# Kernel optimization log

Measured on AMD Instinct MI355X. Metric: run time of the kernel, lower is better.

Reference implementation:

```python
import jax, jax.numpy as jnp
import numpy as np

N_HEAD = 16

def setup_inputs() -> dict:
    key = jax.random.key(0)
    ks = jax.random.split(key, 5)
    B, S, D = 2, 2048, 1024
    x = jax.random.normal(ks[0], (B, S, D), dtype=jnp.float32)
    w_attn = jax.random.normal(ks[1], (3 * D, D), dtype=jnp.float32) * 0.02
    b_attn = jax.random.normal(ks[2], (3 * D,), dtype=jnp.float32) * 0.02
    w_proj = jax.random.normal(ks[3], (D, D), dtype=jnp.float32) * 0.02
    b_proj = jax.random.normal(ks[4], (D,), dtype=jnp.float32) * 0.02
    return {"x": x, "w_attn": w_attn, "b_attn": b_attn, "w_proj": w_proj, "b_proj": b_proj}

def reference(x, w_attn, b_attn, w_proj, b_proj):
    B, S, D = x.shape
    H = N_HEAD
    hd = D // H
    # QKV projection (nn.Linear: x @ W^T + b)
    qkv = x @ w_attn.T + b_attn  # [B, S, 3D]
    q, k, v = jnp.split(qkv, 3, axis=2)
    q = q.reshape(B, S, H, hd).transpose(0, 2, 1, 3)  # [B, H, S, hd]
    k = k.reshape(B, S, H, hd).transpose(0, 2, 1, 3)
    v = v.reshape(B, S, H, hd).transpose(0, 2, 1, 3)
    scale = 1.0 / jnp.sqrt(jnp.asarray(hd, dtype=x.dtype))
    attn = jnp.einsum("bhqd,bhkd->bhqk", q, k) * scale  # [B, H, S, S]
    causal = jnp.tril(jnp.ones((S, S), dtype=bool))
    attn = jnp.where(causal[None, None], attn, -jnp.inf)
    attn = jax.nn.softmax(attn, axis=-1)
    y = jnp.einsum("bhqk,bhkd->bhqd", attn, v)  # [B, H, S, hd]
    y = y.transpose(0, 2, 1, 3).reshape(B, S, D)
    return y @ w_proj.T + b_proj
```

## Files before the change

### kernel.cpp

```cpp
#include <hip/hip_runtime.h>
#include <hip/hip_bf16.h>

#define S_LEN 2048
#define DMODEL 1024
#define NHEAD 16
#define HD 64

typedef short short8 __attribute__((ext_vector_type(8)));
typedef short short4_t __attribute__((ext_vector_type(4)));
typedef float f32x4 __attribute__((ext_vector_type(4)));

#define GLOAD_LDS16(gp, lp)                                        \
    __builtin_amdgcn_global_load_lds(                              \
        (__attribute__((address_space(1))) void*)(gp),             \
        (__attribute__((address_space(3))) void*)(lp), 16, 0, 0)

__device__ inline unsigned short f2bf(float f) {
    union { float f; unsigned int u; } c;
    c.f = f;
    unsigned int r = c.u + 0x7fffu + ((c.u >> 16) & 1u);
    return (unsigned short)(r >> 16);
}

__global__ __launch_bounds__(256) void cast_f32_bf16(
    const float* __restrict__ in, short* __restrict__ out, int n8)
{
    int i = blockIdx.x * 256 + threadIdx.x;
    if (i < n8) {
        float4 a = ((const float4*)in)[2 * i];
        float4 b = ((const float4*)in)[2 * i + 1];
        short8 o;
        o[0] = (short)f2bf(a.x); o[1] = (short)f2bf(a.y);
        o[2] = (short)f2bf(a.z); o[3] = (short)f2bf(a.w);
        o[4] = (short)f2bf(b.x); o[5] = (short)f2bf(b.y);
        o[6] = (short)f2bf(b.z); o[7] = (short)f2bf(b.w);
        ((short8*)out)[i] = o;
    }
}

template<bool QKV>
__global__ __launch_bounds__(256) void gemm_mfma(
    const short* __restrict__ A, const short* __restrict__ W,
    const float* __restrict__ bias, float* __restrict__ C,
    int N, int K,
    short* __restrict__ qo, short* __restrict__ ko, short* __restrict__ vo)
{
    __shared__ __align__(16) short Ash[128 * 64];
    __shared__ __align__(16) short Bsh[128 * 64];

    const int tid = threadIdx.x;
    const int l = tid & 63;
    const int wid = tid >> 6;
    const int wr = wid >> 1, wc = wid & 1;
    const int n0 = blockIdx.x << 7, m0 = blockIdx.y << 7;

    const short* Abase = A + (size_t)m0 * K;
    const short* Wbase = W + (size_t)n0 * K;

    f32x4 acc[4][4];
    #pragma unroll
    for (int i = 0; i < 4; ++i)
        #pragma unroll
        for (int j = 0; j < 4; ++j)
            acc[i][j] = (f32x4)0.0f;

    int rrow[4], scol[4];
    #pragma unroll
    for (int i = 0; i < 4; ++i) {
        int chunk = i * 256 + tid;
        rrow[i] = chunk >> 3;
        scol[i] = ((chunk & 7) ^ (rrow[i] & 7)) << 3;
    }

    const int NT = K >> 6;
    for (int kt = 0; kt < NT; ++kt) {
        const int k0 = kt << 6;
        __syncthreads();
        #pragma unroll
        for (int i = 0; i < 4; ++i) {
            GLOAD_LDS16(Abase + (size_t)rrow[i] * K + k0 + scol[i],
                        &Ash[(i * 256 + wid * 64) * 8]);
            GLOAD_LDS16(Wbase + (size_t)rrow[i] * K + k0 + scol[i],
                        &Bsh[(i * 256 + wid * 64) * 8]);
        }
        __syncthreads();
        #pragma unroll
        for (int kk = 0; kk < 2; ++kk) {
            short8 af[4], bf[4];
            const int slotg = (kk << 2) + (l >> 4);
            #pragma unroll
            for (int mi = 0; mi < 4; ++mi) {
                const int row = wr * 64 + mi * 16 + (l & 15);
                af[mi] = *(const short8*)&Ash[row * 64 + ((slotg ^ (row & 7)) << 3)];
            }
            #pragma unroll
            for (int ni = 0; ni < 4; ++ni) {
                const int row = wc * 64 + ni * 16 + (l & 15);
                bf[ni] = *(const short8*)&Bsh[row * 64 + ((slotg ^ (row & 7)) << 3)];
            }
            #pragma unroll
            for (int mi = 0; mi < 4; ++mi)
                #pragma unroll
                for (int ni = 0; ni < 4; ++ni)
                    acc[mi][ni] = __builtin_amdgcn_mfma_f32_16x16x32_bf16(
                        af[mi], bf[ni], acc[mi][ni], 0, 0, 0);
        }
    }

    #pragma unroll
    for (int ni = 0; ni < 4; ++ni) {
        const int col = n0 + wc * 64 + ni * 16 + (l & 15);
        const float bv = bias[col];
        if (QKV) {
            const int part = col >> 10;
            const int h = (col >> 6) & 15;
            const int e = col & 63;
            short* __restrict__ dst = part == 0 ? qo : (part == 1 ? ko : vo);
            #pragma unroll
            for (int mi = 0; mi < 4; ++mi) {
                #pragma unroll
                for (int r = 0; r < 4; ++r) {
                    int row = m0 + wr * 64 + mi * 16 + ((l >> 4) << 2) + r;
                    int b = row >> 11, s = row & (S_LEN - 1);
                    dst[((size_t)(b * NHEAD + h) * S_LEN + s) * HD + e] =
                        (short)f2bf(acc[mi][ni][r] + bv);
                }
            }
        } else {
            #pragma unroll
            for (int mi = 0; mi < 4; ++mi) {
                #pragma unroll
                for (int r = 0; r < 4; ++r) {
                    int row = m0 + wr * 64 + mi * 16 + ((l >> 4) << 2) + r;
                    C[(size_t)row * N + col] = acc[mi][ni][r] + bv;
                }
            }
        }
    }
}

__global__ __launch_bounds__(256) void transpose_v(
    const short* __restrict__ vin, short* __restrict__ vout)
{
    __shared__ short t[64][72];
    const int tid = threadIdx.x;
    const int bh = blockIdx.x >> 5;
    const int s0 = (blockIdx.x & 31) << 6;
    const size_t ibase = (size_t)bh * S_LEN * HD;
    const size_t obase = (size_t)bh * HD * S_LEN;
    const int r = tid >> 3, c8 = (tid & 7) << 3;

    #pragma unroll
    for (int p = 0; p < 2; ++p) {
        short8 v = *(const short8*)&vin[ibase + (size_t)(s0 + r + p * 32) * HD + c8];
        *(short8*)&t[r + p * 32][c8] = v;
    }
    __syncthreads();
    #pragma unroll
    for (int p = 0; p < 2; ++p) {
        const int e = r + p * 32;
        short8 o;
        #pragma unroll
        for (int i = 0; i < 8; ++i) o[i] = t[c8 + i][e];
        *(short8*)&vout[obase + (size_t)e * S_LEN + s0 + c8] = o;
    }
}

__global__ __launch_bounds__(256) void flash_attn_mfma(
    const short* __restrict__ q, const short* __restrict__ k,
    const short* __restrict__ vt, short* __restrict__ yb)
{
    __shared__ __align__(16) short Ks[64 * 64];
    __shared__ __align__(16) short Vs[64 * 64];

    const int tid = threadIdx.x;
    const int l = tid & 63;
    const int w = tid >> 6;
    const int h4 = l >> 4;
    const int c15 = l & 15;
    const int bid = blockIdx.x;
    const int qt = 31 - (bid >> 5);
    const int bh = bid & 31;
    const int q0 = qt << 6;
    const int myq = q0 + (w << 4) + c15;

    const size_t kbase = (size_t)bh * S_LEN * HD;
    const size_t vbase = (size_t)bh * HD * S_LEN;

    short8 qf[2];
    {
        const short* qrow = q + kbase + (size_t)myq * HD;
        qf[0] = *(const short8*)(qrow + (h4 << 3));
        qf[1] = *(const short8*)(qrow + 32 + (h4 << 3));
    }

    f32x4 accO[4];
    #pragma unroll
    for (int i = 0; i < 4; ++i) accO[i] = (f32x4)0.0f;
    float mr = -1e30f, lr = 0.0f;

    const int sr = tid >> 3, slotL = tid & 7;

    const int ntiles = qt + 1;
    for (int t = 0; t < ntiles; ++t) {
        const int kn = t << 6;
        __syncthreads();
        #pragma unroll
        for (int p = 0; p < 2; ++p) {
            const int row = sr + p * 32;
            const int ss = (slotL ^ (row & 7)) << 3;
            GLOAD_LDS16(k + kbase + (size_t)(kn + row) * HD + ss,
                        &Ks[(p * 256 + w * 64) * 8]);
            GLOAD_LDS16(vt + vbase + (size_t)row * S_LEN + kn + ss,
                        &Vs[(p * 256 + w * 64) * 8]);
        }
        __syncthreads();

        f32x4 sacc[4];
        #pragma unroll
        for (int nt = 0; nt < 4; ++nt) sacc[nt] = (f32x4)0.0f;
        #pragma unroll
        for (int c = 0; c < 2; ++c) {
            const int kof = (c << 5) + (h4 << 3);
            #pragma unroll
            for (int nt = 0; nt < 4; ++nt) {
                const int keyrow = nt * 16 + c15;
                const short8 kf = *(const short8*)&Ks[keyrow * 64 + (kof ^ ((keyrow & 7) << 3))];
                sacc[nt] = __builtin_amdgcn_mfma_f32_16x16x32_bf16(kf, qf[c], sacc[nt], 0, 0, 0);
            }
        }

        float p16[16];
        const bool diag = (t == qt);
        #pragma unroll
        for (int nt = 0; nt < 4; ++nt)
            #pragma unroll
            for (int r = 0; r < 4; ++r) {
                float v = sacc[nt][r] * 0.125f;
                if (diag && (nt * 16 + (h4 << 2) + r > (w << 4) + c15))
                    v = -1e30f;
                p16[nt * 4 + r] = v;
            }

        float mx = p16[0];
        #pragma unroll
        for (int i = 1; i < 16; ++i) mx = fmaxf(mx, p16[i]);
        mx = fmaxf(mx, __shfl_xor(mx, 16, 64));
        mx = fmaxf(mx, __shfl_xor(mx, 32, 64));
        if (!__all(mx <= mr)) {
            const float mnew = fmaxf(mr, mx);
            const float alpha = __expf(mr - mnew);
            mr = mnew;
            lr *= alpha;
            #pragma unroll
            for (int et = 0; et < 4; ++et) accO[et] *= alpha;
        }
        float rs = 0.0f;
        #pragma unroll
        for (int i = 0; i < 16; ++i) {
            p16[i] = __expf(p16[i] - mr);
            rs += p16[i];
        }
        rs += __shfl_xor(rs, 16, 64);
        rs += __shfl_xor(rs, 32, 64);
        lr += rs;

        short8 pb[2];
        #pragma unroll
        for (int c = 0; c < 2; ++c)
            #pragma unroll
            for (int i = 0; i < 8; ++i)
                pb[c][i] = (short)f2bf(p16[8 * c + i]);

        #pragma unroll
        for (int c = 0; c < 2; ++c) {
            const int ch = (c << 2) + (h4 >> 1);
            const int halfo = (h4 & 1) << 2;
            #pragma unroll
            for (int et = 0; et < 4; ++et) {
                const int e = (et << 4) + c15;
                const int rb = e << 6;
                const int sw = e & 7;
                const short4_t va = *(const short4_t*)&Vs[rb + ((ch ^ sw) << 3) + halfo];
                const short4_t vb = *(const short4_t*)&Vs[rb + (((ch + 2) ^ sw) << 3) + halfo];
                const short8 vf = {va[0], va[1], va[2], va[3], vb[0], vb[1], vb[2], vb[3]};
                accO[et] = __builtin_amdgcn_mfma_f32_16x16x32_bf16(vf, pb[c], accO[et], 0, 0, 0);
            }
        }
    }

    const int bq = bh >> 4, hh = bh & 15;
    const float inv = 1.0f / lr;
    short* orow = yb + ((size_t)bq * S_LEN + myq) * DMODEL + hh * HD;
    #pragma unroll
    for (int et = 0; et < 4; ++et) {
        short4_t o;
        #pragma unroll
        for (int r = 0; r < 4; ++r) o[r] = (short)f2bf(accO[et][r] * inv);
        *(short4_t*)&orow[(et << 4) + (h4 << 2)] = o;
    }
}

extern "C" void kernel_launch(void* const* d_in, const int* in_sizes, int n_in,
                              void* d_out, int out_size, void* d_ws, size_t ws_size,
                              hipStream_t stream) {
    const float* x      = (const float*)d_in[0];
    const float* w_attn = (const float*)d_in[1];
    const float* b_attn = (const float*)d_in[2];
    const float* w_proj = (const float*)d_in[3];
    const float* b_proj = (const float*)d_in[4];
    float* out = (float*)d_out;

    const int B = 2;
    const int M = B * S_LEN;
    const size_t x_elems  = (size_t)M * DMODEL;
    const size_t wa_elems = (size_t)3 * DMODEL * DMODEL;
    const size_t wp_elems = (size_t)DMODEL * DMODEL;

    char* wsb = (char*)d_ws;
    short* qw  = (short*)(wsb);
    short* kw  = (short*)(wsb + (8u << 20));
    short* vw  = (short*)(wsb + (16u << 20));
    short* vtw = (short*)(wsb + (24u << 20));
    short* xb  = (short*)(wsb + (32u << 20));
    short* yb  = (short*)(wsb + (32u << 20));
    short* wab = (short*)(wsb + (40u << 20));
    short* wpb = (short*)(wsb + (40u << 20));

    cast_f32_bf16<<<dim3((int)(x_elems  / 8 / 256)), 256, 0, stream>>>(x, xb, (int)(x_elems / 8));
    cast_f32_bf16<<<dim3((int)(wa_elems / 8 / 256)), 256, 0, stream>>>(w_attn, wab, (int)(wa_elems / 8));

    dim3 g1(3 * DMODEL / 128, M / 128);
    gemm_mfma<true><<<g1, 256, 0, stream>>>(xb, wab, b_attn, nullptr,
                                            3 * DMODEL, DMODEL, qw, kw, vw);

    cast_f32_bf16<<<dim3((int)(wp_elems / 8 / 256)), 256, 0, stream>>>(w_proj, wpb, (int)(wp_elems / 8));
    transpose_v<<<dim3(2 * NHEAD * (S_LEN / 64)), 256, 0, stream>>>(vw, vtw);

    flash_attn_mfma<<<dim3(2 * NHEAD * (S_LEN / 64)), 256, 0, stream>>>(qw, kw, vtw, yb);

    dim3 g3(DMODEL / 128, M / 128);
    gemm_mfma<false><<<g3, 256, 0, stream>>>(yb, wpb, b_proj, out,
                                             DMODEL, DMODEL,
                                             nullptr, nullptr, nullptr);
}
```

Measured before the change: 203.9 us.

## Double-buffer LDS in GEMM and flash attention, merge cast kernels

Both the GEMM and the flash-attention kernels now use two LDS buffers. The next K tile is loaded with global_load_lds while the current tile is computed, and the loop drops to one barrier per iteration. The three fp32-to-bf16 cast launches are merged into one kernel that routes each thread by index range, and w_proj gets its own workspace slot. LDS use doubles, which may lower occupancy, and the prefetched loads may not complete before the barrier without an explicit vmcnt wait.

After: 196.5 us. 3.6% less time.

```diff
diff --git a/kernel.cpp b/kernel.cpp
--- a/kernel.cpp
+++ b/kernel.cpp
@@ -22,20 +22,25 @@
     return (unsigned short)(r >> 16);
 }
 
-__global__ __launch_bounds__(256) void cast_f32_bf16(
-    const float* __restrict__ in, short* __restrict__ out, int n8)
+__global__ __launch_bounds__(256) void cast3_f32_bf16(
+    const float* __restrict__ x, const float* __restrict__ wa,
+    const float* __restrict__ wp,
+    short* __restrict__ xb, short* __restrict__ wab, short* __restrict__ wpb)
 {
-    int i = blockIdx.x * 256 + threadIdx.x;
-    if (i < n8) {
-        float4 a = ((const float4*)in)[2 * i];
-        float4 b = ((const float4*)in)[2 * i + 1];
-        short8 o;
-        o[0] = (short)f2bf(a.x); o[1] = (short)f2bf(a.y);
-        o[2] = (short)f2bf(a.z); o[3] = (short)f2bf(a.w);
-        o[4] = (short)f2bf(b.x); o[5] = (short)f2bf(b.y);
-        o[6] = (short)f2bf(b.z); o[7] = (short)f2bf(b.w);
-        ((short8*)out)[i] = o;
-    }
+    const int i = blockIdx.x * 256 + threadIdx.x;
+    const float* src;
+    short* dst;
+    if (i < 524288)      { src = x  + (size_t)i * 8;            dst = xb  + (size_t)i * 8; }
+    else if (i < 917504) { src = wa + (size_t)(i - 524288) * 8; dst = wab + (size_t)(i - 524288) * 8; }
+    else                 { src = wp + (size_t)(i - 917504) * 8; dst = wpb + (size_t)(i - 917504) * 8; }
+    float4 a = ((const float4*)src)[0];
+    float4 b = ((const float4*)src)[1];
+    short8 o;
+    o[0] = (short)f2bf(a.x); o[1] = (short)f2bf(a.y);
+    o[2] = (short)f2bf(a.z); o[3] = (short)f2bf(a.w);
+    o[4] = (short)f2bf(b.x); o[5] = (short)f2bf(b.y);
+    o[6] = (short)f2bf(b.z); o[7] = (short)f2bf(b.w);
+    *(short8*)dst = o;
 }
 
 template<bool QKV>
@@ -45,8 +50,8 @@
     int N, int K,
     short* __restrict__ qo, short* __restrict__ ko, short* __restrict__ vo)
 {
-    __shared__ __align__(16) short Ash[128 * 64];
-    __shared__ __align__(16) short Bsh[128 * 64];
+    __shared__ __align__(16) short Ash[2][128 * 64];
+    __shared__ __align__(16) short Bsh[2][128 * 64];
 
     const int tid = threadIdx.x;
     const int l = tid & 63;
@@ -72,18 +77,17 @@
         scol[i] = ((chunk & 7) ^ (rrow[i] & 7)) << 3;
     }
 
-    const int NT = K >> 6;
-    for (int kt = 0; kt < NT; ++kt) {
-        const int k0 = kt << 6;
-        __syncthreads();
+    auto stage = [&](int buf, int k0) {
         #pragma unroll
         for (int i = 0; i < 4; ++i) {
             GLOAD_LDS16(Abase + (size_t)rrow[i] * K + k0 + scol[i],
-                        &Ash[(i * 256 + wid * 64) * 8]);
+                        &Ash[buf][(i * 256 + wid * 64) * 8]);
             GLOAD_LDS16(Wbase + (size_t)rrow[i] * K + k0 + scol[i],
-                        &Bsh[(i * 256 + wid * 64) * 8]);
-        }
-        __syncthreads();
+                        &Bsh[buf][(i * 256 + wid * 64) * 8]);
+        }
+    };
+
+    auto compute = [&](int buf) {
         #pragma unroll
         for (int kk = 0; kk < 2; ++kk) {
             short8 af[4], bf[4];
@@ -91,12 +95,12 @@
             #pragma unroll
             for (int mi = 0; mi < 4; ++mi) {
                 const int row = wr * 64 + mi * 16 + (l & 15);
-                af[mi] = *(const short8*)&Ash[row * 64 + ((slotg ^ (row & 7)) << 3)];
+                af[mi] = *(const short8*)&Ash[buf][row * 64 + ((slotg ^ (row & 7)) << 3)];
             }
             #pragma unroll
             for (int ni = 0; ni < 4; ++ni) {
                 const int row = wc * 64 + ni * 16 + (l & 15);
-                bf[ni] = *(const short8*)&Bsh[row * 64 + ((slotg ^ (row & 7)) << 3)];
+                bf[ni] = *(const short8*)&Bsh[buf][row * 64 + ((slotg ^ (row & 7)) << 3)];
             }
             #pragma unroll
             for (int mi = 0; mi < 4; ++mi)
@@ -105,6 +109,17 @@
                     acc[mi][ni] = __builtin_amdgcn_mfma_f32_16x16x32_bf16(
                         af[mi], bf[ni], acc[mi][ni], 0, 0, 0);
         }
+    };
+
+    const int NT = K >> 6;
+    stage(0, 0);
+    __syncthreads();
+    int cur = 0;
+    for (int kt = 0; kt < NT; ++kt) {
+        if (kt + 1 < NT) stage(cur ^ 1, (kt + 1) << 6);
+        compute(cur);
+        __syncthreads();
+        cur ^= 1;
     }
 
     #pragma unroll
@@ -170,8 +185,8 @@
     const short* __restrict__ q, const short* __restrict__ k,
     const short* __restrict__ vt, short* __restrict__ yb)
 {
-    __shared__ __align__(16) short Ks[64 * 64];
-    __shared__ __align__(16) short Vs[64 * 64];
+    __shared__ __align__(16) short Ks[2][64 * 64];
+    __shared__ __align__(16) short Vs[2][64 * 64];
 
     const int tid = threadIdx.x;
     const int l = tid & 63;
@@ -201,20 +216,25 @@
 
     const int sr = tid >> 3, slotL = tid & 7;
 
-    const int ntiles = qt + 1;
-    for (int t = 0; t < ntiles; ++t) {
-        const int kn = t << 6;
-        __syncthreads();
+    auto stageKV = [&](int buf, int kn) {
         #pragma unroll
         for (int p = 0; p < 2; ++p) {
             const int row = sr + p * 32;
             const int ss = (slotL ^ (row & 7)) << 3;
             GLOAD_LDS16(k + kbase + (size_t)(kn + row) * HD + ss,
-                        &Ks[(p * 256 + w * 64) * 8]);
+                        &Ks[buf][(p * 256 + w * 64) * 8]);
             GLOAD_LDS16(vt + vbase + (size_t)row * S_LEN + kn + ss,
-                        &Vs[(p * 256 + w * 64) * 8]);
-        }
-        __syncthreads();
+                        &Vs[buf][(p * 256 + w * 64) * 8]);
+        }
+    };
+
+    const int ntiles = qt + 1;
+    stageKV(0, 0);
+    __syncthreads();
+    int cur = 0;
+
+    for (int t = 0; t < ntiles; ++t) {
+        if (t + 1 < ntiles) stageKV(cur ^ 1, (t + 1) << 6);
 
         f32x4 sacc[4];
         #pragma unroll
@@ -225,7 +245,7 @@
             #pragma unroll
             for (int nt = 0; nt < 4; ++nt) {
                 const int keyrow = nt * 16 + c15;
-                const short8 kf = *(const short8*)&Ks[keyrow * 64 + (kof ^ ((keyrow & 7) << 3))];
+                const short8 kf = *(const short8*)&Ks[cur][keyrow * 64 + (kof ^ ((keyrow & 7) << 3))];
                 sacc[nt] = __builtin_amdgcn_mfma_f32_16x16x32_bf16(kf, qf[c], sacc[nt], 0, 0, 0);
             }
         }
@@ -281,12 +301,15 @@
                 const int e = (et << 4) + c15;
                 const int rb = e << 6;
                 const int sw = e & 7;
-                const short4_t va = *(const short4_t*)&Vs[rb + ((ch ^ sw) << 3) + halfo];
-                const short4_t vb = *(const short4_t*)&Vs[rb + (((ch + 2) ^ sw) << 3) + halfo];
+                const short4_t va = *(const short4_t*)&Vs[cur][rb + ((ch ^ sw) << 3) + halfo];
+                const short4_t vb = *(const short4_t*)&Vs[cur][rb + (((ch + 2) ^ sw) << 3) + halfo];
                 const short8 vf = {va[0], va[1], va[2], va[3], vb[0], vb[1], vb[2], vb[3]};
                 accO[et] = __builtin_amdgcn_mfma_f32_16x16x32_bf16(vf, pb[c], accO[et], 0, 0, 0);
             }
         }
+
+        __syncthreads();
+        cur ^= 1;
     }
 
     const int bq = bh >> 4, hh = bh & 15;
@@ -313,9 +336,6 @@
 
     const int B = 2;
     const int M = B * S_LEN;
-    const size_t x_elems  = (size_t)M * DMODEL;
-    const size_t wa_elems = (size_t)3 * DMODEL * DMODEL;
-    const size_t wp_elems = (size_t)DMODEL * DMODEL;
 
     char* wsb = (char*)d_ws;
     short* qw  = (short*)(wsb);
@@ -325,16 +345,14 @@
     short* xb  = (short*)(wsb + (32u << 20));
     short* yb  = (short*)(wsb + (32u << 20));
     short* wab = (short*)(wsb + (40u << 20));
-    short* wpb = (short*)(wsb + (40u << 20));
-
-    cast_f32_bf16<<<dim3((int)(x_elems  / 8 / 256)), 256, 0, stream>>>(x, xb, (int)(x_elems / 8));
-    cast_f32_bf16<<<dim3((int)(wa_elems / 8 / 256)), 256, 0, stream>>>(w_attn, wab, (int)(wa_elems / 8));
+    short* wpb = (short*)(wsb + (46u << 20));
+
+    cast3_f32_bf16<<<dim3(4096), 256, 0, stream>>>(x, w_attn, w_proj, xb, wab, wpb);
 
     dim3 g1(3 * DMODEL / 128, M / 128);
     gemm_mfma<true><<<g1, 256, 0, stream>>>(xb, wab, b_attn, nullptr,
                                             3 * DMODEL, DMODEL, qw, kw, vw);
 
-    cast_f32_bf16<<<dim3((int)(wp_elems / 8 / 256)), 256, 0, stream>>>(w_proj, wpb, (int)(wp_elems / 8));
     transpose_v<<<dim3(2 * NHEAD * (S_LEN / 64)), 256, 0, stream>>>(vw, vtw);
 
     flash_attn_mfma<<<dim3(2 * NHEAD * (S_LEN / 64)), 256, 0, stream>>>(qw, kw, vtw, yb);
```
